# Kernel optimization log

Hardware: AMD Instinct MI355X
Metric: run time of the kernel (lower is better)

Reference implementation:

```python
import jax, jax.numpy as jnp
import numpy as np
from jax import lax

NUM_FILTERS = 180
DN = ('NCHW', 'OIHW', 'NCHW')


def _gabor_kernel(freq, theta, sigma_x, sigma_y, n_stds=3):
    # real part of skimage.filters.gabor_kernel
    ct, st = np.cos(theta), np.sin(theta)
    x0 = int(np.ceil(max(abs(n_stds * sigma_x * ct), abs(n_stds * sigma_y * st), 1)))
    y0 = int(np.ceil(max(abs(n_stds * sigma_y * ct), abs(n_stds * sigma_x * st), 1)))
    y, x = np.mgrid[-y0:y0 + 1, -x0:x0 + 1]
    rotx = x * ct + y * st
    roty = -x * st + y * ct
    g = np.exp(-0.5 * (rotx ** 2 / sigma_x ** 2 + roty ** 2 / sigma_y ** 2))
    g /= 2.0 * np.pi * sigma_x * sigma_y
    return g * np.cos(2.0 * np.pi * freq * rotx)  # Re{exp(1j*2*pi*f*rotx)}


def _make_weights(sigma_x, sigma_y, freq, num_filters):
    kernels = [
        _gabor_kernel(freq, theta=np.pi - th, sigma_x=sigma_x, sigma_y=sigma_y)
        for th in np.linspace(0, np.pi * (num_filters - 1) / num_filters, num_filters)
    ]
    s = max(max(k.shape) for k in kernels)  # 17 for defaults
    kernels = np.stack([
        np.pad(k, [[(s - k.shape[0]) // 2], [(s - k.shape[1]) // 2]]) for k in kernels
    ])
    return kernels.astype(np.float32)


def _gauss1d(sigma, truncate=4.0):
    # matches scipy.ndimage gaussian kernel (skimage default truncate=4.0)
    r = int(truncate * sigma + 0.5)
    xs = np.arange(-r, r + 1, dtype=np.float64)
    k = np.exp(-0.5 * (xs / sigma) ** 2)
    return (k / k.sum()).astype(np.float32), r


def _gaussian_blur(img, sigma):
    # separable blur with edge-replicate ('nearest') padding, img: [B,1,H,W]
    k, r = _gauss1d(sigma)
    kh = jnp.asarray(k).reshape(1, 1, -1, 1)
    kw = jnp.asarray(k).reshape(1, 1, 1, -1)
    p = jnp.pad(img, ((0, 0), (0, 0), (r, r), (0, 0)), mode='edge')
    img = lax.conv_general_dilated(p, kh, (1, 1), 'VALID', dimension_numbers=DN)
    p = jnp.pad(img, ((0, 0), (0, 0), (0, 0), (r, r)), mode='edge')
    return lax.conv_general_dilated(p, kw, (1, 1), 'VALID', dimension_numbers=DN)


def setup_inputs() -> dict:
    key = jax.random.key(0)
    x = jax.random.uniform(key, (2, 3, 512, 512), dtype=jnp.float32)
    weights = jnp.asarray(_make_weights(1.8, 2.4, 0.23, NUM_FILTERS))[:, None, :, :]  # [180,1,17,17]
    bins = jnp.asarray(
        np.linspace(0, np.pi * (NUM_FILTERS - 1) / NUM_FILTERS, NUM_FILTERS), jnp.float32
    ).reshape(1, -1, 1, 1)
    return {'x': x, 'weights': weights, 'bins': bins}


def reference(x, weights, bins):
    # rgb -> gray, [B,1,H,W]
    gray = (0.2989 * x[:, 0] + 0.587 * x[:, 1] + 0.114 * x[:, 2])[:, None]
    # difference of gaussians (skimage, low=0.4, high=10.0)
    filtered = _gaussian_blur(gray, 0.4) - _gaussian_blur(gray, 10.0)
    kh, kw = weights.shape[2], weights.shape[3]
    response = lax.conv_general_dilated(
        filtered, weights, (1, 1), ((kh // 2, kh // 2), (kw // 2, kw // 2)),
        dimension_numbers=DN)  # [B,180,H,W]
    response = jnp.abs(response)
    idx = jnp.argmax(response, axis=1)[:, None]  # [B,1,H,W]
    orientation_map = idx.astype(jnp.float32) / NUM_FILTERS * 255.0
    orientation_map_rad = orientation_map / NUM_FILTERS * jnp.pi
    d0 = jnp.abs(orientation_map_rad - bins)
    dists = jnp.minimum(d0, jnp.minimum(jnp.abs(orientation_map_rad - bins - jnp.pi),
                                        jnp.abs(orientation_map_rad - bins + jnp.pi)))
    F_orients_norm = response / jnp.sum(response, axis=1, keepdims=True)
    confidence_map = jnp.sum(dists ** 2 * F_orients_norm, axis=1)  # [B,H,W]
    return orientation_map, confidence_map
```

## Files before the change

### kernel.cpp

```cpp
#include <hip/hip_runtime.h>
#include <math.h>
#include <stdint.h>

#define H 512
#define W 512
#define NPIX (H * W)
#define NB 2
#define NF 180
#define KS 17
#define WSCALE 1024.0f

#define RAW_OFF 0
#define BB_OFF  1440
#define BCH_U32 3072
#define PH_U32  (2 * BCH_U32)
#define POOL_U32 (1440 + 2 * PH_U32)

typedef _Float16 half8 __attribute__((ext_vector_type(8)));
typedef float floatx16 __attribute__((ext_vector_type(16)));
typedef uint32_t u32x4 __attribute__((ext_vector_type(4)));

union FragU { u32x4 u; half8 h; };

__device__ inline void gl_lds16(const uint32_t* g, uint32_t* l) {
  __builtin_amdgcn_global_load_lds((const __attribute__((address_space(1))) void*)g,
                                   (__attribute__((address_space(3))) void*)l, 16, 0, 0);
}

__global__ void k_taps(float* __restrict__ taps) {
  if (threadIdx.x == 0 && blockIdx.x == 0) {
    {
      double k[5], s = 0.0;
      for (int i = 0; i < 5; i++) { double xv = (double)(i - 2) / 0.4; k[i] = exp(-0.5 * xv * xv); s += k[i]; }
      for (int i = 0; i < 5; i++) taps[i] = (float)(k[i] / s);
    }
    {
      double k[81], s = 0.0;
      for (int i = 0; i < 81; i++) { double xv = (double)(i - 40) / 10.0; k[i] = exp(-0.5 * xv * xv); s += k[i]; }
      for (int i = 0; i < 81; i++) taps[8 + i] = (float)(k[i] / s);
    }
  }
}

__global__ void k_repackB(const float* __restrict__ w, uint32_t* __restrict__ Bf) {
  int tid = blockIdx.x * 256 + threadIdx.x;
  if (tid >= 19 * 6 * 64 * 4) return;
  int q = tid & 3;
  int lane = (tid >> 2) & 63;
  int ct = tid >> 8;
  int t = ct % 6, c = ct / 6;
  int n = t * 32 + (lane & 31);
  int hf = lane >> 5;
  uint32_t hv = 0, lv = 0;
  for (int s = 0; s < 2; s++) {
    int j = 2 * q + s;
    int k = hf * 8 + j;
    float val = 0.f;
    if (n < NF) {
      if (c < 17)       val = w[n * 289 + c * 17 + k];
      else if (c == 17) val = w[n * 289 + k * 17 + 16];
      else if (k == 0)  val = w[n * 289 + 16 * 17 + 16];
    }
    val *= WSCALE;
    _Float16 hh = (_Float16)val;
    _Float16 ll = (_Float16)(val - (float)hh);
    hv |= (uint32_t)__builtin_bit_cast(uint16_t, hh) << (16 * s);
    lv |= (uint32_t)__builtin_bit_cast(uint16_t, ll) << (16 * s);
  }
  int base = c * 3072;
  int off = t * 256 + lane * 4 + q;
  Bf[base + off] = hv;
  Bf[base + 1536 + off] = lv;
}

__global__ void k_gray(const float* __restrict__ x, float* __restrict__ gray) {
  int i = blockIdx.x * blockDim.x + threadIdx.x;
  if (i >= NB * NPIX) return;
  int b = i / NPIX, r = i % NPIX;
  const float* xb = x + (size_t)b * 3 * NPIX;
  gray[i] = 0.2989f * xb[r] + 0.587f * xb[NPIX + r] + 0.114f * xb[2 * NPIX + r];
}

__global__ void k_vblur2(const float* __restrict__ in, float* __restrict__ outA,
                         float* __restrict__ outB, const float* __restrict__ taps) {
  int i = blockIdx.x * blockDim.x + threadIdx.x;
  if (i >= NB * NPIX) return;
  int b = i / NPIX, r = i % NPIX;
  int y = r / W, xx = r % W;
  const float* img = in + (size_t)b * NPIX;
  float a = 0.f;
#pragma unroll
  for (int j = -2; j <= 2; j++) {
    int yy = y + j; yy = yy < 0 ? 0 : (yy > H - 1 ? H - 1 : yy);
    a = fmaf(taps[j + 2], img[yy * W + xx], a);
  }
  float c = 0.f;
  for (int j = -40; j <= 40; j++) {
    int yy = y + j; yy = yy < 0 ? 0 : (yy > H - 1 ? H - 1 : yy);
    c = fmaf(taps[8 + j + 40], img[yy * W + xx], c);
  }
  outA[i] = a;
  outB[i] = c;
}

__global__ void k_hblur_dog(const float* __restrict__ inA, const float* __restrict__ inB,
                            uint32_t* __restrict__ dogp, const float* __restrict__ taps) {
  int i = blockIdx.x * blockDim.x + threadIdx.x;
  if (i >= NB * NPIX) return;
  int b = i / NPIX, r = i % NPIX;
  int y = r / W, xx = r % W;
  const float* ra = inA + (size_t)b * NPIX + (size_t)y * W;
  const float* rb = inB + (size_t)b * NPIX + (size_t)y * W;
  float a = 0.f;
#pragma unroll
  for (int j = -2; j <= 2; j++) {
    int xc = xx + j; xc = xc < 0 ? 0 : (xc > W - 1 ? W - 1 : xc);
    a = fmaf(taps[j + 2], ra[xc], a);
  }
  float c = 0.f;
  for (int j = -40; j <= 40; j++) {
    int xc = xx + j; xc = xc < 0 ? 0 : (xc > W - 1 ? W - 1 : xc);
    c = fmaf(taps[8 + j + 40], rb[xc], c);
  }
  float d = a - c;
  _Float16 hh = (_Float16)d;
  _Float16 ll = (_Float16)(d - (float)hh);
  dogp[i] = ((uint32_t)__builtin_bit_cast(uint16_t, ll) << 16) |
            (uint32_t)__builtin_bit_cast(uint16_t, hh);
}

__launch_bounds__(256, 2)
__global__ void k_conv(const uint32_t* __restrict__ dogp,
                       const uint32_t* __restrict__ Bf,
                       const float* __restrict__ bins,
                       float* __restrict__ out) {
  __shared__ uint32_t pool[POOL_U32];

  const int b  = blockIdx.z;
  const int y0 = blockIdx.y * 2;
  const int x0 = blockIdx.x * 64;
  const int tid = threadIdx.x;
  const int lane = tid & 63;
  const int w  = __builtin_amdgcn_readfirstlane(tid >> 6);
  const int fg  = w & 1;
  const int ch  = w >> 1;
  const int nl = lane & 31;
  const int half = lane >> 5;

  const uint32_t* dgb = dogp + (size_t)b * NPIX;
  for (int i = tid; i < 18 * 80; i += 256) {
    int ry = i / 80, rx = i % 80;
    int gy = y0 + ry - 8, gx = x0 + rx - 8;
    uint32_t v = 0;
    if (gy >= 0 && gy < H && gx >= 0 && gx < W) v = dgb[gy * W + gx];
    pool[RAW_OFF + i] = v;
  }
  {
    const uint32_t* src = Bf + (size_t)tid * 4;
    uint32_t* dst = &pool[BB_OFF + tid * 4];
#pragma unroll
    for (int i = 0; i < 6; i++) gl_lds16(src + i * 1024, dst + i * 1024);
  }
  asm volatile("s_waitcnt vmcnt(0)" ::: "memory");
  __syncthreads();

  floatx16 acc[2][3];
#pragma unroll
  for (int d = 0; d < 2; d++)
#pragma unroll
    for (int t = 0; t < 3; t++)
#pragma unroll
      for (int q = 0; q < 16; q++) acc[d][t][q] = 0.f;

  const int abase = ch * 32 + nl + half * 8;

  auto buildRow = [&](int tr, FragU& fh, FragU& fl) {
    const uint32_t* rp = &pool[RAW_OFF + tr * 80 + abase];
    uint32_t d[8];
#pragma unroll
    for (int j = 0; j < 8; j++) d[j] = rp[j];
#pragma unroll
    for (int q = 0; q < 4; q++) {
      fh.u[q] = __builtin_amdgcn_perm(d[2 * q + 1], d[2 * q], 0x05040100u);
      fl.u[q] = __builtin_amdgcn_perm(d[2 * q + 1], d[2 * q], 0x07060302u);
    }
  };
  auto buildStrip = [&](int c, int rb, FragU& fh, FragU& fl) {
    int kyb = (c - 17) * 16 + half * 8;
    uint32_t d[8];
#pragma unroll
    for (int j = 0; j < 8; j++) {
      int ky = kyb + j; if (ky > 16) ky = 16;
      d[j] = pool[RAW_OFF + (rb + ky) * 80 + ch * 32 + nl + 16];
    }
#pragma unroll
    for (int q = 0; q < 4; q++) {
      fh.u[q] = __builtin_amdgcn_perm(d[2 * q + 1], d[2 * q], 0x05040100u);
      fl.u[q] = __builtin_amdgcn_perm(d[2 * q + 1], d[2 * q], 0x07060302u);
    }
  };
  auto mfmaChunk = [&](int off, FragU& d0h, FragU& d0l, FragU& d1h, FragU& d1l) {
    FragU wh[3], wl[3];
#pragma unroll
    for (int t = 0; t < 3; t++) {
      wh[t].u = *(const u32x4*)&pool[off + (3 * fg + t) * 256 + lane * 4];
      wl[t].u = *(const u32x4*)&pool[off + 1536 + (3 * fg + t) * 256 + lane * 4];
    }
#pragma unroll
    for (int t = 0; t < 3; t++) {
      acc[0][t] = __builtin_amdgcn_mfma_f32_32x32x16_f16(wh[t].h, d0h.h, acc[0][t], 0, 0, 0);
      acc[1][t] = __builtin_amdgcn_mfma_f32_32x32x16_f16(wh[t].h, d1h.h, acc[1][t], 0, 0, 0);
    }
#pragma unroll
    for (int t = 0; t < 3; t++) {
      acc[0][t] = __builtin_amdgcn_mfma_f32_32x32x16_f16(wh[t].h, d0l.h, acc[0][t], 0, 0, 0);
      acc[1][t] = __builtin_amdgcn_mfma_f32_32x32x16_f16(wh[t].h, d1l.h, acc[1][t], 0, 0, 0);
    }
#pragma unroll
    for (int t = 0; t < 3; t++) {
      acc[0][t] = __builtin_amdgcn_mfma_f32_32x32x16_f16(wl[t].h, d0h.h, acc[0][t], 0, 0, 0);
      acc[1][t] = __builtin_amdgcn_mfma_f32_32x32x16_f16(wl[t].h, d1h.h, acc[1][t], 0, 0, 0);
    }
  };

  FragU a0h, a0l, a1h, a1l;
  buildRow(0, a0h, a0l);

  int buf = 0;
  for (int p = 0; p < 8; p++) {
    {
      const uint32_t* src = Bf + (size_t)(2 * p + 2) * BCH_U32 + (size_t)tid * 4;
      uint32_t* dst = &pool[BB_OFF + (buf ^ 1) * PH_U32 + tid * 4];
#pragma unroll
      for (int i = 0; i < 6; i++) gl_lds16(src + i * 1024, dst + i * 1024);
    }
    buildRow(1 + 2 * p, a1h, a1l);
    mfmaChunk(BB_OFF + buf * PH_U32, a0h, a0l, a1h, a1l);
    a0h = a1h; a0l = a1l;
    buildRow(2 + 2 * p, a1h, a1l);
    mfmaChunk(BB_OFF + buf * PH_U32 + BCH_U32, a0h, a0l, a1h, a1l);
    a0h = a1h; a0l = a1l;

    asm volatile("s_waitcnt vmcnt(0)" ::: "memory");
    __syncthreads();
    buf ^= 1;
  }

  {
    const uint32_t* src = Bf + (size_t)18 * BCH_U32 + (size_t)tid * 4;
    uint32_t* dst = &pool[BB_OFF + (buf ^ 1) * PH_U32 + tid * 4];
#pragma unroll
    for (int i = 0; i < 3; i++) gl_lds16(src + i * 1024, dst + i * 1024);

    buildRow(17, a1h, a1l);
    mfmaChunk(BB_OFF + buf * PH_U32, a0h, a0l, a1h, a1l);

    FragU s0h, s0l, s1h, s1l;
    buildStrip(17, 0, s0h, s0l);
    buildStrip(17, 1, s1h, s1l);
    mfmaChunk(BB_OFF + buf * PH_U32 + BCH_U32, s0h, s0l, s1h, s1l);

    asm volatile("s_waitcnt vmcnt(0)" ::: "memory");
    __syncthreads();
    buf ^= 1;
  }
  {
    FragU s0h, s0l, s1h, s1l;
    buildStrip(18, 0, s0h, s0l);
    buildStrip(18, 1, s1h, s1l);
    mfmaChunk(BB_OFF + buf * PH_U32, s0h, s0l, s1h, s1l);
  }
  __syncthreads();

  float* pm = (float*)&pool[0];
  int*   pn = (int*)&pool[256];
  float* pS = (float*)&pool[512];
  float* pc = (float*)&pool[768];
  int*   fn = (int*)&pool[1024];
  float* fS = (float*)&pool[1152];

  const float PI_F = 3.14159265358979323846f;
  const float INV_PI = 0.31830988618379067154f;
  const double STEPD = 3.14159265358979323846 * 179.0 / 180.0 / 179.0;
  const float stepf = (float)STEPD;
  const float hbase = (4.0f * (float)half) * stepf;
  const int colp = ch * 32 + nl;

#pragma unroll
  for (int d = 0; d < 2; d++) {
    float m = -1.f; int n = 0; float S0 = 0.f, S1 = 0.f;
#pragma unroll
    for (int t = 0; t < 3; t++) {
#pragma unroll
      for (int q = 0; q < 16; q++) {
        float v = fabsf(acc[d][t][q]);
        if (q & 1) S1 += v; else S0 += v;
        int nf = 32 * (3 * fg + t) + (q & 3) + 8 * (q >> 2) + 4 * half;
        if (v > m) { m = v; n = nf; }
      }
    }
    float S = S0 + S1;
    float mo = __shfl_xor(m, 32);
    int   no = __shfl_xor(n, 32);
    float So = __shfl_xor(S, 32);
    bool take = (mo > m) || (mo == m && no < n);
    if (take) { m = mo; n = no; }
    S += So;
    if (half == 0) {
      int o = (d * 2 + fg) * 64 + colp;
      pm[o] = m; pn[o] = n; pS[o] = S;
    }
  }
  __syncthreads();

  if (fg == 0) {
#pragma unroll
    for (int d = 0; d < 2; d++) {
      int o0 = (d * 2 + 0) * 64 + colp;
      int o1 = (d * 2 + 1) * 64 + colp;
      float m0 = pm[o0], m1 = pm[o1];
      int n = (m1 > m0) ? pn[o1] : pn[o0];
      float S = pS[o0] + pS[o1];
      float om = (float)n / 180.0f * 255.0f;
      if (half == 0) {
        fn[d * 64 + colp] = n; fS[d * 64 + colp] = S;
        out[(size_t)b * NPIX + (size_t)(y0 + d) * W + x0 + colp] = om;
      }
    }
  }
  __syncthreads();

#pragma unroll
  for (int d = 0; d < 2; d++) {
    int nwin = fn[d * 64 + colp];
    float om = (float)nwin / 180.0f * 255.0f;
    float rad = om / 180.0f * PI_F;
    float ddc = rad - hbase;
    float C0 = 0.f, C1 = 0.f;
#pragma unroll
    for (int t = 0; t < 3; t++) {
#pragma unroll
      for (int q = 0; q < 16; q++) {
        const float K = (float)((double)(32 * (3 * fg + t) + (q & 3) + 8 * (q >> 2)) * STEPD);
        float dd = ddc - K;
        float r = rintf(dd * INV_PI);
        float dist = fmaf(-PI_F, r, dd);
        float w2 = dist * dist;
        if (q & 1) C1 = fmaf(w2, fabsf(acc[d][t][q]), C1);
        else       C0 = fmaf(w2, fabsf(acc[d][t][q]), C0);
      }
    }
    float C = C0 + C1;
    C += __shfl_xor(C, 32);
    if (half == 0) pc[(d * 2 + fg) * 64 + colp] = C;
  }
  __syncthreads();

  if (fg == 0) {
#pragma unroll
    for (int d = 0; d < 2; d++) {
      float C = pc[(d * 2 + 0) * 64 + colp] + pc[(d * 2 + 1) * 64 + colp];
      if (half == 0) {
        out[(size_t)NB * NPIX + (size_t)b * NPIX + (size_t)(y0 + d) * W + x0 + colp]
            = C / fS[d * 64 + colp];
      }
    }
  }
}

extern "C" void kernel_launch(void* const* d_in, const int* in_sizes, int n_in,
                              void* d_out, int out_size, void* d_ws, size_t ws_size,
                              hipStream_t stream) {
  const float* x = (const float*)d_in[0];
  const float* wts = (const float*)d_in[1];
  const float* bins = (const float*)d_in[2];
  float* out = (float*)d_out;

  float* ws = (float*)d_ws;
  float* gray = ws;
  float* tmpA = ws + (size_t)NB * NPIX;
  float* tmpB = tmpA + (size_t)NB * NPIX;
  uint32_t* dogp = (uint32_t*)(tmpB + (size_t)NB * NPIX);
  float* taps = (float*)(dogp + (size_t)NB * NPIX);
  uint32_t* Bf = (uint32_t*)(taps + 128);

  k_taps<<<1, 64, 0, stream>>>(taps);
  k_repackB<<<114, 256, 0, stream>>>(wts, Bf);

  int n = NB * NPIX;
  int blk = 256, grd = (n + blk - 1) / blk;
  k_gray<<<grd, blk, 0, stream>>>(x, gray);
  k_vblur2<<<grd, blk, 0, stream>>>(gray, tmpA, tmpB, taps);
  k_hblur_dog<<<grd, blk, 0, stream>>>(tmpA, tmpB, dogp, taps);

  dim3 g(W / 64, H / 2, NB);
  k_conv<<<g, 256, 0, stream>>>(dogp, Bf, bins, out);
}
```

Measured before the change: 195.6 us.

## Load Gabor weight fragments directly from global into registers, drop LDS staging

Weight fragments are no longer staged through double-buffered LDS with async global-to-LDS copies and per-chunk barriers. Each wave now prefetches its own weight fragments for the next chunk straight from global memory (L2-cached) into registers while doing the current chunk's MFMAs. This removes the in-loop __syncthreads and shrinks LDS to the raw tile, which may allow more resident blocks. The cost is more redundant global/L2 traffic across blocks, extra VGPRs for the prefetch buffers, and load latency exposed to each wave.

```diff
diff --git a/kernel.cpp b/kernel.cpp
--- a/kernel.cpp
+++ b/kernel.cpp
@@ -10,22 +10,14 @@
 #define KS 17
 #define WSCALE 1024.0f
 
-#define RAW_OFF 0
-#define BB_OFF  1440
+#define RAW_U32 1440
 #define BCH_U32 3072
-#define PH_U32  (2 * BCH_U32)
-#define POOL_U32 (1440 + 2 * PH_U32)
 
 typedef _Float16 half8 __attribute__((ext_vector_type(8)));
 typedef float floatx16 __attribute__((ext_vector_type(16)));
 typedef uint32_t u32x4 __attribute__((ext_vector_type(4)));
 
 union FragU { u32x4 u; half8 h; };
-
-__device__ inline void gl_lds16(const uint32_t* g, uint32_t* l) {
-  __builtin_amdgcn_global_load_lds((const __attribute__((address_space(1))) void*)g,
-                                   (__attribute__((address_space(3))) void*)l, 16, 0, 0);
-}
 
 __global__ void k_taps(float* __restrict__ taps) {
   if (threadIdx.x == 0 && blockIdx.x == 0) {
@@ -134,7 +126,7 @@
                        const uint32_t* __restrict__ Bf,
                        const float* __restrict__ bins,
                        float* __restrict__ out) {
-  __shared__ uint32_t pool[POOL_U32];
+  __shared__ uint32_t pool[RAW_U32];
 
   const int b  = blockIdx.z;
   const int y0 = blockIdx.y * 2;
@@ -153,15 +145,8 @@
     int gy = y0 + ry - 8, gx = x0 + rx - 8;
     uint32_t v = 0;
     if (gy >= 0 && gy < H && gx >= 0 && gx < W) v = dgb[gy * W + gx];
-    pool[RAW_OFF + i] = v;
-  }
-  {
-    const uint32_t* src = Bf + (size_t)tid * 4;
-    uint32_t* dst = &pool[BB_OFF + tid * 4];
-#pragma unroll
-    for (int i = 0; i < 6; i++) gl_lds16(src + i * 1024, dst + i * 1024);
-  }
-  asm volatile("s_waitcnt vmcnt(0)" ::: "memory");
+    pool[i] = v;
+  }
   __syncthreads();
 
   floatx16 acc[2][3];
@@ -175,7 +160,7 @@
   const int abase = ch * 32 + nl + half * 8;
 
   auto buildRow = [&](int tr, FragU& fh, FragU& fl) {
-    const uint32_t* rp = &pool[RAW_OFF + tr * 80 + abase];
+    const uint32_t* rp = &pool[tr * 80 + abase];
     uint32_t d[8];
 #pragma unroll
     for (int j = 0; j < 8; j++) d[j] = rp[j];
@@ -191,7 +176,7 @@
 #pragma unroll
     for (int j = 0; j < 8; j++) {
       int ky = kyb + j; if (ky > 16) ky = 16;
-      d[j] = pool[RAW_OFF + (rb + ky) * 80 + ch * 32 + nl + 16];
+      d[j] = pool[(rb + ky) * 80 + ch * 32 + nl + 16];
     }
 #pragma unroll
     for (int q = 0; q < 4; q++) {
@@ -199,13 +184,8 @@
       fl.u[q] = __builtin_amdgcn_perm(d[2 * q + 1], d[2 * q], 0x07060302u);
     }
   };
-  auto mfmaChunk = [&](int off, FragU& d0h, FragU& d0l, FragU& d1h, FragU& d1l) {
-    FragU wh[3], wl[3];
-#pragma unroll
-    for (int t = 0; t < 3; t++) {
-      wh[t].u = *(const u32x4*)&pool[off + (3 * fg + t) * 256 + lane * 4];
-      wl[t].u = *(const u32x4*)&pool[off + 1536 + (3 * fg + t) * 256 + lane * 4];
-    }
+  auto mfma18 = [&](FragU* wh, FragU* wl,
+                    FragU& d0h, FragU& d0l, FragU& d1h, FragU& d1l) {
 #pragma unroll
     for (int t = 0; t < 3; t++) {
       acc[0][t] = __builtin_amdgcn_mfma_f32_32x32x16_f16(wh[t].h, d0h.h, acc[0][t], 0, 0, 0);
@@ -223,52 +203,53 @@
     }
   };
 
+  const uint32_t* wbh = Bf + (size_t)(3 * fg) * 256 + (size_t)lane * 4;
+  const uint32_t* wbl = wbh + 1536;
+
+  FragU wch[3], wcl[3], wnh[3], wnl2[3];
+#pragma unroll
+  for (int t = 0; t < 3; t++) {
+    wch[t].u = *(const u32x4*)(wbh + t * 256);
+    wcl[t].u = *(const u32x4*)(wbl + t * 256);
+  }
+
   FragU a0h, a0l, a1h, a1l;
   buildRow(0, a0h, a0l);
 
-  int buf = 0;
-  for (int p = 0; p < 8; p++) {
-    {
-      const uint32_t* src = Bf + (size_t)(2 * p + 2) * BCH_U32 + (size_t)tid * 4;
-      uint32_t* dst = &pool[BB_OFF + (buf ^ 1) * PH_U32 + tid * 4];
-#pragma unroll
-      for (int i = 0; i < 6; i++) gl_lds16(src + i * 1024, dst + i * 1024);
-    }
-    buildRow(1 + 2 * p, a1h, a1l);
-    mfmaChunk(BB_OFF + buf * PH_U32, a0h, a0l, a1h, a1l);
+  for (int c = 0; c < 17; c++) {
+    const uint32_t* nbh = wbh + (size_t)(c + 1) * BCH_U32;
+    const uint32_t* nbl = wbl + (size_t)(c + 1) * BCH_U32;
+#pragma unroll
+    for (int t = 0; t < 3; t++) {
+      wnh[t].u  = *(const u32x4*)(nbh + t * 256);
+      wnl2[t].u = *(const u32x4*)(nbl + t * 256);
+    }
+    buildRow(c + 1, a1h, a1l);
+    mfma18(wch, wcl, a0h, a0l, a1h, a1l);
     a0h = a1h; a0l = a1l;
-    buildRow(2 + 2 * p, a1h, a1l);
-    mfmaChunk(BB_OFF + buf * PH_U32 + BCH_U32, a0h, a0l, a1h, a1l);
-    a0h = a1h; a0l = a1l;
-
-    asm volatile("s_waitcnt vmcnt(0)" ::: "memory");
-    __syncthreads();
-    buf ^= 1;
-  }
-
+#pragma unroll
+    for (int t = 0; t < 3; t++) { wch[t] = wnh[t]; wcl[t] = wnl2[t]; }
+  }
   {
-    const uint32_t* src = Bf + (size_t)18 * BCH_U32 + (size_t)tid * 4;
-    uint32_t* dst = &pool[BB_OFF + (buf ^ 1) * PH_U32 + tid * 4];
-#pragma unroll
-    for (int i = 0; i < 3; i++) gl_lds16(src + i * 1024, dst + i * 1024);
-
-    buildRow(17, a1h, a1l);
-    mfmaChunk(BB_OFF + buf * PH_U32, a0h, a0l, a1h, a1l);
-
+    const uint32_t* nbh = wbh + (size_t)18 * BCH_U32;
+    const uint32_t* nbl = wbl + (size_t)18 * BCH_U32;
+#pragma unroll
+    for (int t = 0; t < 3; t++) {
+      wnh[t].u  = *(const u32x4*)(nbh + t * 256);
+      wnl2[t].u = *(const u32x4*)(nbl + t * 256);
+    }
     FragU s0h, s0l, s1h, s1l;
     buildStrip(17, 0, s0h, s0l);
     buildStrip(17, 1, s1h, s1l);
-    mfmaChunk(BB_OFF + buf * PH_U32 + BCH_U32, s0h, s0l, s1h, s1l);
-
-    asm volatile("s_waitcnt vmcnt(0)" ::: "memory");
-    __syncthreads();
-    buf ^= 1;
+    mfma18(wch, wcl, s0h, s0l, s1h, s1l);
+#pragma unroll
+    for (int t = 0; t < 3; t++) { wch[t] = wnh[t]; wcl[t] = wnl2[t]; }
   }
   {
     FragU s0h, s0l, s1h, s1l;
     buildStrip(18, 0, s0h, s0l);
     buildStrip(18, 1, s1h, s1l);
-    mfmaChunk(BB_OFF + buf * PH_U32, s0h, s0l, s1h, s1l);
+    mfma18(wch, wcl, s0h, s0l, s1h, s1l);
   }
   __syncthreads();
 
```

Measured after the change: 191.5 us. 1.02x faster.
